# Kernel optimization log

Measured on AMD Instinct MI355X. Metric: run time of the kernel, lower is better.

## Reference

```python
import jax, jax.numpy as jnp
import numpy as np

N_NODES = 100000
N_EDGES = 1600000
D = 128


def sage_conv(x, src, dst, W_l, b_l, W_r):
    # mean aggregation of neighbor features: messages flow src -> dst
    msgs = x[src]                                           # [E, D] gather
    agg = jax.ops.segment_sum(msgs, dst, num_segments=x.shape[0])  # [N, D]
    deg = jax.ops.segment_sum(jnp.ones((src.shape[0],), x.dtype), dst,
                              num_segments=x.shape[0])       # [N]
    agg = agg / jnp.maximum(deg, 1.0)[:, None]
    # PyG SAGEConv: lin_l(aggregated) + lin_r(root); bias lives in lin_l
    return agg @ W_l.T + b_l + x @ W_r.T


def setup_inputs() -> dict:
    key = jax.random.key(0)
    ks = jax.random.split(key, 8)
    s = 1.0 / np.sqrt(D)
    return {
        "x": jax.random.normal(ks[0], (N_NODES, D), dtype=jnp.float32),
        "edge_index": jax.random.randint(ks[1], (2, N_EDGES), 0, N_NODES, dtype=jnp.int64),
        "W1_l": jax.random.normal(ks[2], (D, D), dtype=jnp.float32) * s,
        "b1": jnp.zeros((D,), dtype=jnp.float32),
        "W1_r": jax.random.normal(ks[3], (D, D), dtype=jnp.float32) * s,
        "W2_l": jax.random.normal(ks[4], (D, D), dtype=jnp.float32) * s,
        "b2": jnp.zeros((D,), dtype=jnp.float32),
        "W2_r": jax.random.normal(ks[5], (D, D), dtype=jnp.float32) * s,
    }


def reference(x, edge_index, W1_l, b1, W1_r, W2_l, b2, W2_r):
    src, dst = edge_index[0], edge_index[1]
    h = jax.nn.relu(sage_conv(x, src, dst, W1_l, b1, W1_r))
    out = sage_conv(h, src, dst, W2_l, b2, W2_r)
    return out
```

## Files before the change

### kernel.cpp

```cpp
#include <hip/hip_runtime.h>
#include <cstdint>
#include <cstddef>

#define D 128

typedef unsigned short ushort_t;
typedef unsigned int uint_t;
typedef __attribute__((ext_vector_type(8))) short bf16x8;
typedef __attribute__((ext_vector_type(4))) float f32x4;

static __device__ __forceinline__ unsigned short f2bf(float f) {
    unsigned int u = __float_as_uint(f);
    u = (u + 0x7FFFu + ((u >> 16) & 1u)) >> 16;
    return (unsigned short)u;
}
static __device__ __forceinline__ float bf_lo(uint_t v) {
    return __uint_as_float(v << 16);
}
static __device__ __forceinline__ float bf_hi(uint_t v) {
    return __uint_as_float(v & 0xFFFF0000u);
}


__global__ __launch_bounds__(256) void bkt_hist(const int* __restrict__ dst,
                                                int* __restrict__ bhist, int E) {
    __shared__ int lh[512];
    int t = threadIdx.x;
    lh[t] = 0;
    lh[t + 256] = 0;
    __syncthreads();
    int base = blockIdx.x * 4096;
#pragma unroll
    for (int i = 0; i < 16; ++i) {
        int e = base + i * 256 + t;
        if (e < E) atomicAdd(&lh[dst[e] >> 8], 1);
    }
    __syncthreads();
    if (lh[t]) atomicAdd(&bhist[t], lh[t]);
    if (lh[t + 256]) atomicAdd(&bhist[t + 256], lh[t + 256]);
}

__global__ __launch_bounds__(512) void bkt_scan(const int* __restrict__ bhist,
                                                int* __restrict__ boff,
                                                int* __restrict__ bcur,
                                                int* __restrict__ row_ptr,
                                                int N, int E) {
    __shared__ int s[512];
    int t = threadIdx.x;
    int v = bhist[t];
    s[t] = v;
    __syncthreads();
    for (int off = 1; off < 512; off <<= 1) {
        int u = (t >= off) ? s[t - off] : 0;
        __syncthreads();
        s[t] += u;
        __syncthreads();
    }
    int ex = s[t] - v;
    boff[t] = ex;
    bcur[t] = ex;
    if (t == 511) boff[512] = s[511];
    if (t == 0) row_ptr[N] = E;
}

__global__ __launch_bounds__(256) void bkt_scatter(const int* __restrict__ src,
                                                   const int* __restrict__ dst,
                                                   int* __restrict__ bcur,
                                                   int* __restrict__ ebuf, int E) {
    __shared__ int lh[512];
    __shared__ int gb[512];
    int t = threadIdx.x;
    lh[t] = 0;
    lh[t + 256] = 0;
    __syncthreads();
    int base = blockIdx.x * 4096;
    unsigned pk[16];
#pragma unroll
    for (int i = 0; i < 16; ++i) {
        int e = base + i * 256 + t;
        unsigned p = 0xFFFFFFFFu;
        if (e < E) {
            int d = dst[e];
            int bkt = d >> 8;
            int r = atomicAdd(&lh[bkt], 1);
            p = ((unsigned)r << 17) | ((unsigned)bkt << 8) | (unsigned)(d & 255);
        }
        pk[i] = p;
    }
    __syncthreads();
    if (lh[t]) gb[t] = atomicAdd(&bcur[t], lh[t]);
    if (lh[t + 256]) gb[t + 256] = atomicAdd(&bcur[t + 256], lh[t + 256]);
    __syncthreads();
#pragma unroll
    for (int i = 0; i < 16; ++i) {
        int e = base + i * 256 + t;
        if (e < E) {
            unsigned p = pk[i];
            int bkt = (p >> 8) & 511;
            int r = (int)(p >> 17);
            ebuf[gb[bkt] + r] = src[e] | ((int)(p & 255) << 20);
        }
    }
}

__global__ __launch_bounds__(256) void bkt_build(const int* __restrict__ ebuf,
                                                 const int* __restrict__ boff,
                                                 int* __restrict__ row_ptr,
                                                 int* __restrict__ csr, int N) {
    __shared__ int lcnt[256];
    __shared__ int lofs[256];
    __shared__ int lcur[256];
    int t = threadIdx.x;
    int b = blockIdx.x;
    int base = b << 8;
    int ebeg = boff[b], eend = boff[b + 1];
    lcnt[t] = 0;
    __syncthreads();
    for (int e = ebeg + t; e < eend; e += 256)
        atomicAdd(&lcnt[((unsigned)ebuf[e]) >> 20], 1);
    __syncthreads();
    int v = lcnt[t];
    lofs[t] = v;
    __syncthreads();
    for (int off = 1; off < 256; off <<= 1) {
        int u = (t >= off) ? lofs[t - off] : 0;
        __syncthreads();
        lofs[t] += u;
        __syncthreads();
    }
    int ex = lofs[t] - v;
    __syncthreads();
    lofs[t] = ex;
    lcur[t] = 0;
    if (base + t < N) row_ptr[base + t] = ebeg + ex;
    __syncthreads();
    for (int e = ebeg + t; e < eend; e += 256) {
        int u = ebuf[e];
        int d = ((unsigned)u) >> 20;
        int r = atomicAdd(&lcur[d], 1);
        csr[ebeg + lofs[d] + r] = u & 0xFFFFF;
    }
}


__global__ __launch_bounds__(256) void cast_x_kernel(const float* __restrict__ src,
                                                     ushort_t* __restrict__ dst,
                                                     long n) {
    long i = ((long)blockIdx.x * 256 + threadIdx.x) * 8;
    if (i >= n) return;
    float4 a = *(const float4*)(src + i);
    float4 b = *(const float4*)(src + i + 4);
    uint4 o;
    o.x = (uint_t)f2bf(a.x) | ((uint_t)f2bf(a.y) << 16);
    o.y = (uint_t)f2bf(a.z) | ((uint_t)f2bf(a.w) << 16);
    o.z = (uint_t)f2bf(b.x) | ((uint_t)f2bf(b.y) << 16);
    o.w = (uint_t)f2bf(b.z) | ((uint_t)f2bf(b.w) << 16);
    *(uint4*)(dst + i) = o;
}

__global__ __launch_bounds__(256) void cast_w_kernel(const float* __restrict__ s0,
                                                     const float* __restrict__ s1,
                                                     const float* __restrict__ s2,
                                                     const float* __restrict__ s3,
                                                     ushort_t* __restrict__ d0,
                                                     ushort_t* __restrict__ d1,
                                                     ushort_t* __restrict__ d2,
                                                     ushort_t* __restrict__ d3) {
    const float* s = (blockIdx.y == 0) ? s0 : (blockIdx.y == 1) ? s1
                   : (blockIdx.y == 2) ? s2 : s3;
    ushort_t* d = (blockIdx.y == 0) ? d0 : (blockIdx.y == 1) ? d1
                : (blockIdx.y == 2) ? d2 : d3;
    long i = ((long)blockIdx.x * 256 + threadIdx.x) * 8;
    float4 a = *(const float4*)(s + i);
    float4 b = *(const float4*)(s + i + 4);
    uint4 o;
    o.x = (uint_t)f2bf(a.x) | ((uint_t)f2bf(a.y) << 16);
    o.y = (uint_t)f2bf(a.z) | ((uint_t)f2bf(a.w) << 16);
    o.z = (uint_t)f2bf(b.x) | ((uint_t)f2bf(b.y) << 16);
    o.w = (uint_t)f2bf(b.z) | ((uint_t)f2bf(b.w) << 16);
    *(uint4*)(d + i) = o;
}


__global__ __launch_bounds__(256) void agg_b_kernel(const ushort_t* __restrict__ xin,
                                                    const int* __restrict__ csr,
                                                    const int* __restrict__ row_ptr,
                                                    ushort_t* __restrict__ aggb, int N) {
    int node = blockIdx.x * 4 + (threadIdx.x >> 6);
    if (node >= N) return;
    int lane = threadIdx.x & 63;
    int half = lane >> 5;
    int l32 = lane & 31;
    int beg = row_ptr[node], end = row_ptr[node + 1];
    int deg = end - beg;
    float a0 = 0.f, a1 = 0.f, a2 = 0.f, a3 = 0.f;
    int e = beg;
    for (; e + 16 <= end; e += 16) {
        uint2 v[8];
#pragma unroll
        for (int q = 0; q < 8; ++q) {
            int s = csr[e + 2 * q + half];
            v[q] = ((const uint2*)(xin + (size_t)s * D))[l32];
        }
#pragma unroll
        for (int q = 0; q < 8; ++q) {
            a0 += bf_lo(v[q].x); a1 += bf_hi(v[q].x);
            a2 += bf_lo(v[q].y); a3 += bf_hi(v[q].y);
        }
    }
    if (e + 8 <= end) {
        uint2 v[4];
#pragma unroll
        for (int q = 0; q < 4; ++q) {
            int s = csr[e + 2 * q + half];
            v[q] = ((const uint2*)(xin + (size_t)s * D))[l32];
        }
#pragma unroll
        for (int q = 0; q < 4; ++q) {
            a0 += bf_lo(v[q].x); a1 += bf_hi(v[q].x);
            a2 += bf_lo(v[q].y); a3 += bf_hi(v[q].y);
        }
        e += 8;
    }
    if (e + 4 <= end) {
        uint2 v[2];
#pragma unroll
        for (int q = 0; q < 2; ++q) {
            int s = csr[e + 2 * q + half];
            v[q] = ((const uint2*)(xin + (size_t)s * D))[l32];
        }
#pragma unroll
        for (int q = 0; q < 2; ++q) {
            a0 += bf_lo(v[q].x); a1 += bf_hi(v[q].x);
            a2 += bf_lo(v[q].y); a3 += bf_hi(v[q].y);
        }
        e += 4;
    }
    if (e + 2 <= end) {
        int s = csr[e + half];
        uint2 v = ((const uint2*)(xin + (size_t)s * D))[l32];
        a0 += bf_lo(v.x); a1 += bf_hi(v.x);
        a2 += bf_lo(v.y); a3 += bf_hi(v.y);
        e += 2;
    }
    if (e < end && half == 0) {
        int s = csr[e];
        uint2 v = ((const uint2*)(xin + (size_t)s * D))[l32];
        a0 += bf_lo(v.x); a1 += bf_hi(v.x);
        a2 += bf_lo(v.y); a3 += bf_hi(v.y);
    }
    a0 += __shfl_xor(a0, 32, 64);
    a1 += __shfl_xor(a1, 32, 64);
    a2 += __shfl_xor(a2, 32, 64);
    a3 += __shfl_xor(a3, 32, 64);
    if (half == 0) {
        float inv = 1.0f / fmaxf((float)deg, 1.0f);
        uint2 o;
        o.x = (uint_t)f2bf(a0 * inv) | ((uint_t)f2bf(a1 * inv) << 16);
        o.y = (uint_t)f2bf(a2 * inv) | ((uint_t)f2bf(a3 * inv) << 16);
        ((uint2*)(aggb + (size_t)node * D))[l32] = o;
    }
}


__global__ __launch_bounds__(256) void gemm_mfma(const ushort_t* __restrict__ Aagg,
                                                 const ushort_t* __restrict__ Ax,
                                                 const ushort_t* __restrict__ Wl,
                                                 const ushort_t* __restrict__ Wr,
                                                 const float* __restrict__ bias,
                                                 ushort_t* __restrict__ out_bf,
                                                 float* __restrict__ out_f32,
                                                 int N, int relu_bf) {
    __shared__ ushort_t sA[128 * 32];
    __shared__ ushort_t sW[128 * 32];
    int tid = threadIdx.x;
    int wave = tid >> 6, lane = tid & 63;
    int quad = lane >> 4, l15 = lane & 15;
    int wm = wave & 1, wc = wave >> 1;
    int n0 = blockIdx.x * 128;

    int sr = tid >> 2;
    int sseg = (tid & 3) * 8;

    f32x4 acc[4][4];
#pragma unroll
    for (int mt = 0; mt < 4; ++mt)
#pragma unroll
        for (int nt = 0; nt < 4; ++nt) acc[mt][nt] = (f32x4){0.f, 0.f, 0.f, 0.f};

    int ga0 = min(n0 + sr, N - 1);
    int ga1 = min(n0 + sr + 64, N - 1);

#pragma unroll
    for (int c = 0; c < 8; ++c) {
        const ushort_t* Ab = (c < 4) ? Aagg : Ax;
        const ushort_t* Wb = (c < 4) ? Wl : Wr;
        int koff = (c & 3) * 32 + sseg;
        bf16x8 va0 = *(const bf16x8*)(Ab + (size_t)ga0 * D + koff);
        bf16x8 va1 = *(const bf16x8*)(Ab + (size_t)ga1 * D + koff);
        bf16x8 vw0 = *(const bf16x8*)(Wb + (size_t)sr * D + koff);
        bf16x8 vw1 = *(const bf16x8*)(Wb + (size_t)(sr + 64) * D + koff);
        __syncthreads();
        *(bf16x8*)&sA[sr * 32 + sseg] = va0;
        *(bf16x8*)&sA[(sr + 64) * 32 + sseg] = va1;
        *(bf16x8*)&sW[sr * 32 + sseg] = vw0;
        *(bf16x8*)&sW[(sr + 64) * 32 + sseg] = vw1;
        __syncthreads();

        bf16x8 af[4], wf[4];
#pragma unroll
        for (int mt = 0; mt < 4; ++mt)
            af[mt] = *(const bf16x8*)&sA[(wm * 64 + mt * 16 + l15) * 32 + quad * 8];
#pragma unroll
        for (int nt = 0; nt < 4; ++nt)
            wf[nt] = *(const bf16x8*)&sW[(wc * 64 + nt * 16 + l15) * 32 + quad * 8];
#pragma unroll
        for (int mt = 0; mt < 4; ++mt)
#pragma unroll
            for (int nt = 0; nt < 4; ++nt)
                acc[mt][nt] = __builtin_amdgcn_mfma_f32_16x16x32_bf16(
                    af[mt], wf[nt], acc[mt][nt], 0, 0, 0);
    }

#pragma unroll
    for (int mt = 0; mt < 4; ++mt) {
#pragma unroll
        for (int nt = 0; nt < 4; ++nt) {
            int col = wc * 64 + nt * 16 + l15;
            float bv = bias[col];
#pragma unroll
            for (int reg = 0; reg < 4; ++reg) {
                int row = n0 + wm * 64 + mt * 16 + quad * 4 + reg;
                if (row < N) {
                    float v = acc[mt][nt][reg] + bv;
                    if (relu_bf) {
                        v = fmaxf(v, 0.f);
                        out_bf[(size_t)row * D + col] = f2bf(v);
                    } else {
                        out_f32[(size_t)row * D + col] = v;
                    }
                }
            }
        }
    }
}


extern "C" void kernel_launch(void* const* d_in, const int* in_sizes, int n_in,
                              void* d_out, int out_size, void* d_ws, size_t ws_size,
                              hipStream_t stream) {
    const float* x   = (const float*)d_in[0];
    const int*   ei  = (const int*)d_in[1];
    const float* W1l = (const float*)d_in[2];
    const float* b1  = (const float*)d_in[3];
    const float* W1r = (const float*)d_in[4];
    const float* W2l = (const float*)d_in[5];
    const float* b2  = (const float*)d_in[6];
    const float* W2r = (const float*)d_in[7];
    float* out = (float*)d_out;

    int N = in_sizes[0] / D;
    int E = in_sizes[1] / 2;
    const int* src = ei;
    const int* dst = ei + E;

    char* ws = (char*)d_ws;
    size_t off = 0;
    auto take = [&](size_t bytes) -> char* {
        char* p = ws + off;
        off += (bytes + 255) & ~(size_t)255;
        return p;
    };
    int*      row_ptr = (int*)take((size_t)(N + 1) * sizeof(int));
    int*      bhist   = (int*)take((size_t)(512 + 512 + 513) * sizeof(int));
    int*      bcur    = bhist + 512;
    int*      boff    = bhist + 1024;
    int*      ebuf    = (int*)take((size_t)E * sizeof(int));
    int*      csr     = (int*)take((size_t)E * sizeof(int));
    ushort_t* xb      = (ushort_t*)take((size_t)N * D * sizeof(ushort_t));
    ushort_t* hb      = (ushort_t*)take((size_t)N * D * sizeof(ushort_t));
    ushort_t* aggb    = (ushort_t*)take((size_t)N * D * sizeof(ushort_t));
    ushort_t* W1lb    = (ushort_t*)take((size_t)D * D * sizeof(ushort_t));
    ushort_t* W1rb    = (ushort_t*)take((size_t)D * D * sizeof(ushort_t));
    ushort_t* W2lb    = (ushort_t*)take((size_t)D * D * sizeof(ushort_t));
    ushort_t* W2rb    = (ushort_t*)take((size_t)D * D * sizeof(ushort_t));
    (void)ws_size;
    (void)n_in;
    (void)out_size;

    hipMemsetAsync(bhist, 0, 1024 * sizeof(int), stream);

    int NB = (N + 255) / 256;
    int EB = (E + 4095) / 4096;

    bkt_hist<<<EB, 256, 0, stream>>>(dst, bhist, E);
    bkt_scan<<<1, 512, 0, stream>>>(bhist, boff, bcur, row_ptr, N, E);
    bkt_scatter<<<EB, 256, 0, stream>>>(src, dst, bcur, ebuf, E);
    bkt_build<<<NB, 256, 0, stream>>>(ebuf, boff, row_ptr, csr, N);

    long nx = (long)N * D;
    cast_x_kernel<<<(int)((nx / 8 + 255) / 256), 256, 0, stream>>>(x, xb, nx);
    cast_w_kernel<<<dim3(8, 4), 256, 0, stream>>>(W1l, W1r, W2l, W2r,
                                                  W1lb, W1rb, W2lb, W2rb);

    int ablocks = (N + 3) / 4;
    int gblocks = (N + 127) / 128;

    agg_b_kernel<<<ablocks, 256, 0, stream>>>(xb, csr, row_ptr, aggb, N);
    gemm_mfma<<<gblocks, 256, 0, stream>>>(aggb, xb, W1lb, W1rb, b1, hb, nullptr, N, 1);

    agg_b_kernel<<<ablocks, 256, 0, stream>>>(hb, csr, row_ptr, aggb, N);
    gemm_mfma<<<gblocks, 256, 0, stream>>>(aggb, hb, W2lb, W2rb, b2, nullptr, out, N, 0);
}
```

Measured before the change: 347.5 us.

## Rework neighbor aggregation: 16-byte row loads, 4 edges per wave, shuffled indices

The aggregation kernel now has each 16-lane group load a full bf16 feature row with 16-byte loads, so a wave gathers four neighbor rows at once instead of two. Neighbor indices are loaded once per wave (one per lane) and broadcast with shuffles rather than re-read from memory per edge. Row addresses use 32-bit offset arithmetic. This is meant to raise memory-level parallelism and cut index-load traffic in the gather, in exchange for an extra cross-group reduction step and a 32-bit offset that relies on node count times row size fitting in unsigned range.

```diff
diff --git a/kernel.cpp b/kernel.cpp
--- a/kernel.cpp
+++ b/kernel.cpp
@@ -182,6 +182,19 @@
 }
 
 
+static __device__ __forceinline__ void acc8(uint4 v, float a[8]) {
+    a[0] += bf_lo(v.x); a[1] += bf_hi(v.x);
+    a[2] += bf_lo(v.y); a[3] += bf_hi(v.y);
+    a[4] += bf_lo(v.z); a[5] += bf_hi(v.z);
+    a[6] += bf_lo(v.w); a[7] += bf_hi(v.w);
+}
+
+static __device__ __forceinline__ uint4 grow(const ushort_t* __restrict__ xin,
+                                             int s, int l16) {
+    unsigned off = ((unsigned)s << 8) | ((unsigned)l16 << 4);
+    return *(const uint4*)((const char*)xin + off);
+}
+
 __global__ __launch_bounds__(256) void agg_b_kernel(const ushort_t* __restrict__ xin,
                                                     const int* __restrict__ csr,
                                                     const int* __restrict__ row_ptr,
@@ -189,76 +202,62 @@
     int node = blockIdx.x * 4 + (threadIdx.x >> 6);
     if (node >= N) return;
     int lane = threadIdx.x & 63;
-    int half = lane >> 5;
-    int l32 = lane & 31;
+    int g = lane >> 4;
+    int l16 = lane & 15;
     int beg = row_ptr[node], end = row_ptr[node + 1];
     int deg = end - beg;
-    float a0 = 0.f, a1 = 0.f, a2 = 0.f, a3 = 0.f;
-    int e = beg;
-    for (; e + 16 <= end; e += 16) {
-        uint2 v[8];
-#pragma unroll
-        for (int q = 0; q < 8; ++q) {
-            int s = csr[e + 2 * q + half];
-            v[q] = ((const uint2*)(xin + (size_t)s * D))[l32];
-        }
-#pragma unroll
-        for (int q = 0; q < 8; ++q) {
-            a0 += bf_lo(v[q].x); a1 += bf_hi(v[q].x);
-            a2 += bf_lo(v[q].y); a3 += bf_hi(v[q].y);
-        }
-    }
-    if (e + 8 <= end) {
-        uint2 v[4];
-#pragma unroll
-        for (int q = 0; q < 4; ++q) {
-            int s = csr[e + 2 * q + half];
-            v[q] = ((const uint2*)(xin + (size_t)s * D))[l32];
-        }
-#pragma unroll
-        for (int q = 0; q < 4; ++q) {
-            a0 += bf_lo(v[q].x); a1 += bf_hi(v[q].x);
-            a2 += bf_lo(v[q].y); a3 += bf_hi(v[q].y);
-        }
-        e += 8;
-    }
-    if (e + 4 <= end) {
-        uint2 v[2];
-#pragma unroll
-        for (int q = 0; q < 2; ++q) {
-            int s = csr[e + 2 * q + half];
-            v[q] = ((const uint2*)(xin + (size_t)s * D))[l32];
-        }
-#pragma unroll
-        for (int q = 0; q < 2; ++q) {
-            a0 += bf_lo(v[q].x); a1 += bf_hi(v[q].x);
-            a2 += bf_lo(v[q].y); a3 += bf_hi(v[q].y);
-        }
-        e += 4;
-    }
-    if (e + 2 <= end) {
-        int s = csr[e + half];
-        uint2 v = ((const uint2*)(xin + (size_t)s * D))[l32];
-        a0 += bf_lo(v.x); a1 += bf_hi(v.x);
-        a2 += bf_lo(v.y); a3 += bf_hi(v.y);
-        e += 2;
-    }
-    if (e < end && half == 0) {
-        int s = csr[e];
-        uint2 v = ((const uint2*)(xin + (size_t)s * D))[l32];
-        a0 += bf_lo(v.x); a1 += bf_hi(v.x);
-        a2 += bf_lo(v.y); a3 += bf_hi(v.y);
-    }
-    a0 += __shfl_xor(a0, 32, 64);
-    a1 += __shfl_xor(a1, 32, 64);
-    a2 += __shfl_xor(a2, 32, 64);
-    a3 += __shfl_xor(a3, 32, 64);
-    if (half == 0) {
+    float a[8] = {0.f, 0.f, 0.f, 0.f, 0.f, 0.f, 0.f, 0.f};
+
+    if (deg > 0) {
+        int deg64 = min(deg, 64);
+        int myidx = csr[beg + min(lane, deg - 1)];
+        int e = 0;
+        for (; e + 16 <= deg64; e += 16) {
+            int s0 = __shfl(myidx, e + g);
+            int s1 = __shfl(myidx, e + 4 + g);
+            int s2 = __shfl(myidx, e + 8 + g);
+            int s3 = __shfl(myidx, e + 12 + g);
+            uint4 v0 = grow(xin, s0, l16);
+            uint4 v1 = grow(xin, s1, l16);
+            uint4 v2 = grow(xin, s2, l16);
+            uint4 v3 = grow(xin, s3, l16);
+            acc8(v0, a); acc8(v1, a); acc8(v2, a); acc8(v3, a);
+        }
+        if (e + 8 <= deg64) {
+            int s0 = __shfl(myidx, e + g);
+            int s1 = __shfl(myidx, e + 4 + g);
+            uint4 v0 = grow(xin, s0, l16);
+            uint4 v1 = grow(xin, s1, l16);
+            acc8(v0, a); acc8(v1, a);
+            e += 8;
+        }
+        for (; e < deg64; e += 4) {
+            int ee = min(e + g, deg64 - 1);
+            int s = __shfl(myidx, ee);
+            uint4 v = grow(xin, s, l16);
+            if (e + g < deg64) acc8(v, a);
+        }
+        for (int e2 = 64; e2 < deg; e2 += 4) {
+            int s = csr[beg + min(e2 + g, deg - 1)];
+            uint4 v = grow(xin, s, l16);
+            if (e2 + g < deg) acc8(v, a);
+        }
+    }
+
+#pragma unroll
+    for (int i = 0; i < 8; ++i) {
+        a[i] += __shfl_xor(a[i], 16);
+        a[i] += __shfl_xor(a[i], 32);
+    }
+    if (g == 0) {
         float inv = 1.0f / fmaxf((float)deg, 1.0f);
-        uint2 o;
-        o.x = (uint_t)f2bf(a0 * inv) | ((uint_t)f2bf(a1 * inv) << 16);
-        o.y = (uint_t)f2bf(a2 * inv) | ((uint_t)f2bf(a3 * inv) << 16);
-        ((uint2*)(aggb + (size_t)node * D))[l32] = o;
+        uint4 o;
+        o.x = (uint_t)f2bf(a[0] * inv) | ((uint_t)f2bf(a[1] * inv) << 16);
+        o.y = (uint_t)f2bf(a[2] * inv) | ((uint_t)f2bf(a[3] * inv) << 16);
+        o.z = (uint_t)f2bf(a[4] * inv) | ((uint_t)f2bf(a[5] * inv) << 16);
+        o.w = (uint_t)f2bf(a[6] * inv) | ((uint_t)f2bf(a[7] * inv) << 16);
+        unsigned off = ((unsigned)node << 8) | ((unsigned)l16 << 4);
+        *(uint4*)((char*)aggb + off) = o;
     }
 }
 
```

Result: faster. 335.0 us (-3.6%).
